# Performance work log

Hardware: AMD Instinct MI355X
Metric: run time of the kernel (lower is better)

The kernel has to match this reference:

```python
import jax, jax.numpy as jnp
import numpy as np

B, H, L, P = 16, 256, 8192, 64  # batch, d_input, seq_len, d_state


def setup_inputs() -> dict:
    key = jax.random.key(0)
    k1, k2, k3, k4, k5, k6 = jax.random.split(key, 6)
    u = jax.random.normal(k1, (B, H, L), dtype=jnp.float32)
    # diagonal SSM poles on an annulus inside the unit disk (stable discrete dynamics)
    radius = jax.random.uniform(k2, (P,), minval=0.5, maxval=0.99)
    theta = jax.random.uniform(k3, (P,), minval=0.0, maxval=2.0 * np.pi)
    A_re = (radius * jnp.cos(theta)).astype(jnp.float32)
    A_im = (radius * jnp.sin(theta)).astype(jnp.float32)
    # combined input/output mixing W = C*B, complex (H, P)
    BC_re = (jax.random.normal(k4, (H, P)) / np.sqrt(P)).astype(jnp.float32)
    BC_im = (jax.random.normal(k5, (H, P)) / np.sqrt(P)).astype(jnp.float32)
    # D skip vector: uniform_ring(min_radius=0.0, max_radius=1.0, field='real')
    D = jax.random.uniform(k6, (H,), minval=0.0, maxval=1.0, dtype=jnp.float32)
    return {"u": u, "A_re": A_re, "A_im": A_im, "BC_re": BC_re, "BC_im": BC_im, "D": D}


def reference(u, A_re, A_im, BC_re, BC_im, D):
    # Vandermonde kernel: k[h, l] = sum_p BC[h, p] * A[p]**l, computed stably via exp(l*log A)
    A = jax.lax.complex(A_re, A_im)                      # (P,)
    logA = jnp.log(A)                                    # (P,) complex
    ell = jnp.arange(L, dtype=jnp.float32)               # (L,)
    V = jnp.exp(logA[:, None] * ell[None, :])            # (P, L) complex Vandermonde
    BC = jax.lax.complex(BC_re, BC_im)                   # (H, P)
    k = jnp.einsum('hp,pl->hl', BC, V)                   # (H, L) complex kernel
    # circular FFT convolution (same-length fft/ifft as the torch code)
    u_s = jnp.fft.fft(u, axis=-1)                        # (B, H, L) complex
    k_s = jnp.fft.fft(k, axis=-1)                        # (H, L) complex
    y = jnp.fft.ifft(u_s * k_s[None, :, :], axis=-1).real
    y = y + D[None, :, None] * u                         # D*u skip
    return jnp.tanh(y)                                   # activation (dropout=0 -> identity)
```

## Files before the change

### kernel.cpp

```cpp
#include <hip/hip_runtime.h>
#include <cmath>


typedef _Float16 half8 __attribute__((ext_vector_type(8)));
typedef _Float16 half4v __attribute__((ext_vector_type(4)));
typedef float floatx16 __attribute__((ext_vector_type(16)));

#define NC 64
#define CM 128
#define ROWP 136
#define A2_BYTES ((size_t)256 * 128 * 256 * 2)
#define W_BYTES  ((size_t)128 * 128 * 2)
#define AM_OFF   (A2_BYTES + W_BYTES)

__device__ __forceinline__ float fast_tanh(float x) {
    float e2 = __expf(2.0f * x);
    return 1.0f - 2.0f / (e2 + 1.0f);
}

__global__ void fftconv_prep(const float* __restrict__ A_re, const float* __restrict__ A_im,
                             const float* __restrict__ BC_re, const float* __restrict__ BC_im,
                             const float* __restrict__ Dv, char* __restrict__ ws) {
    __shared__ float rr[64], th[64], br[64], bi[64];
    __shared__ float kk[CM];
    const int h = blockIdx.x, tid = threadIdx.x;
    if (tid < 64) {
        float x = A_re[tid], y = A_im[tid];
        rr[tid] = log2f(sqrtf(x * x + y * y));
        th[tid] = atan2f(y, x);
        br[tid] = BC_re[h * 64 + tid];
        bi[tid] = BC_im[h * 64 + tid];
    }
    __syncthreads();
    if (tid < CM) {
        float d = (float)tid, s = 0.f;
        for (int p = 0; p < 64; ++p) {
            float mag = exp2f(d * rr[p]);
            float ang = d * th[p];
            s += mag * (br[p] * cosf(ang) - bi[p] * sinf(ang));
        }
        kk[tid] = s;
    }
    __syncthreads();
    _Float16* A2 = (_Float16*)ws + (size_t)h * 128 * 256;
    const float Dh = Dv[h];
    for (int idx = tid; idx < 128 * 128; idx += 256) {
        int r = idx >> 7, pc = idx & 127, p = pc & 63;
        float e = (float)(r + 1);
        float mag = exp2f(e * rr[p]);
        float ang = e * th[p];
        float cr = mag * cosf(ang), ci = mag * sinf(ang);
        float val = (pc < 64) ? (br[p] * cr - bi[p] * ci) : -(br[p] * ci + bi[p] * cr);
        A2[r * 256 + pc] = (_Float16)val;
    }
    for (int idx = tid; idx < 128 * 128; idx += 256) {
        int r = idx >> 7, j = idx & 127;
        float v = (j <= r) ? kk[r - j] : 0.f;
        if (j == r) v += Dh;
        A2[r * 256 + CM + j] = (_Float16)v;
    }
    if (h == 0) {
        _Float16* W = (_Float16*)(ws + A2_BYTES);
        for (int idx = tid; idx < 128 * 128; idx += 256) {
            int pc = idx >> 7, j = idx & 127, p = pc & 63;
            float e = (float)(127 - j);
            float mag = exp2f(e * rr[p]);
            float ang = e * th[p];
            float v = (pc < 64) ? mag * cosf(ang) : mag * sinf(ang);
            W[pc * 128 + j] = (_Float16)v;
        }
        if (tid < 64) {
            float mag = exp2f(128.f * rr[tid]);
            float ang = 128.f * th[tid];
            float* aM = (float*)(ws + AM_OFF);
            aM[tid] = mag * cosf(ang);
            aM[64 + tid] = mag * sinf(ang);
        }
    }
}

__global__ __launch_bounds__(256, 2)
void fftconv_main(const float* __restrict__ u, const char* __restrict__ ws,
                  float* __restrict__ out) {
    __shared__ __align__(16) _Float16 u16p[NC * ROWP];
    __shared__ __align__(16) _Float16 S16[NC * ROWP];

    const int tid = threadIdx.x;
    const int lane = tid & 63;
    const int wv = tid >> 6;
    const int h = blockIdx.x >> 4;
    const int bb = blockIdx.x & 15;
    const float* ub = u + ((size_t)bb * 256 + h) * 8192;
    float* yb = out + ((size_t)bb * 256 + h) * 8192;

#pragma unroll
    for (int i = 0; i < 8; ++i) {
        int e4 = i * 256 + tid;
        float4 v = ((const float4*)ub)[e4];
        int el = e4 << 2;
        int c = el >> 7, j = el & 127;
        half4v hv = { (_Float16)v.x, (_Float16)v.y, (_Float16)v.z, (_Float16)v.w };
        *(half4v*)&u16p[c * ROWP + j] = hv;
    }
    __syncthreads();

    const int mrow = (wv << 5) + (lane & 31);
    const int kh = (lane >> 5) << 3;
    const int ncol = lane & 31;

    {
        const _Float16* Wg = (const _Float16*)(ws + A2_BYTES);
        floatx16 acc0 = {}; floatx16 acc1 = {};
#pragma unroll
        for (int s = 0; s < 8; ++s) {
            int k0 = (s << 4) + kh;
            half8 af = *(const half8*)(Wg + mrow * CM + k0);
            half8 b0 = *(const half8*)&u16p[ncol * ROWP + k0];
            half8 b1 = *(const half8*)&u16p[(ncol + 32) * ROWP + k0];
            acc0 = __builtin_amdgcn_mfma_f32_32x32x16_f16(af, b0, acc0, 0, 0, 0);
            acc1 = __builtin_amdgcn_mfma_f32_32x32x16_f16(af, b1, acc1, 0, 0, 0);
        }
        const int pc0 = (wv << 5) + ((lane >> 5) << 2);
#pragma unroll
        for (int g = 0; g < 4; ++g) {
            half4v h0 = { (_Float16)acc0[4 * g + 0], (_Float16)acc0[4 * g + 1],
                          (_Float16)acc0[4 * g + 2], (_Float16)acc0[4 * g + 3] };
            *(half4v*)&S16[ncol * ROWP + pc0 + 8 * g] = h0;
            half4v h1 = { (_Float16)acc1[4 * g + 0], (_Float16)acc1[4 * g + 1],
                          (_Float16)acc1[4 * g + 2], (_Float16)acc1[4 * g + 3] };
            *(half4v*)&S16[(ncol + 32) * ROWP + pc0 + 8 * g] = h1;
        }
    }
    __syncthreads();

    if (wv == 0) {
        const float* aM = (const float*)(ws + AM_OFF);
        const float amr = aM[lane], ami = aM[64 + lane];
        float sr = 0.f, si = 0.f;
#pragma unroll
        for (int c = NC - 8; c < NC; ++c) {
            float xr = (float)S16[c * ROWP + lane];
            float xi = (float)S16[c * ROWP + 64 + lane];
            float nr = fmaf(amr, sr, fmaf(-ami, si, xr));
            float ni = fmaf(amr, si, fmaf(ami, sr, xi));
            sr = nr; si = ni;
        }
#pragma unroll
        for (int c = 0; c < NC; ++c) {
            float xr = (float)S16[c * ROWP + lane];
            float xi = (float)S16[c * ROWP + 64 + lane];
            S16[c * ROWP + lane] = (_Float16)sr;
            S16[c * ROWP + 64 + lane] = (_Float16)si;
            float nr = fmaf(amr, sr, fmaf(-ami, si, xr));
            float ni = fmaf(amr, si, fmaf(ami, sr, xi));
            sr = nr; si = ni;
        }
    }
    __syncthreads();

    {
        const _Float16* Ag = (const _Float16*)ws + ((size_t)h * CM + mrow) * 256;
        floatx16 acc0 = {}; floatx16 acc1 = {};
#pragma unroll
        for (int s = 0; s < 8; ++s) {
            int k0 = (s << 4) + kh;
            half8 af = *(const half8*)(Ag + k0);
            half8 b0 = *(const half8*)&S16[ncol * ROWP + k0];
            half8 b1 = *(const half8*)&S16[(ncol + 32) * ROWP + k0];
            acc0 = __builtin_amdgcn_mfma_f32_32x32x16_f16(af, b0, acc0, 0, 0, 0);
            acc1 = __builtin_amdgcn_mfma_f32_32x32x16_f16(af, b1, acc1, 0, 0, 0);
        }
#pragma unroll
        for (int s = 0; s < 8; ++s) {
            int k0 = (s << 4) + kh;
            half8 af = *(const half8*)(Ag + CM + k0);
            half8 b0 = *(const half8*)&u16p[ncol * ROWP + k0];
            half8 b1 = *(const half8*)&u16p[(ncol + 32) * ROWP + k0];
            acc0 = __builtin_amdgcn_mfma_f32_32x32x16_f16(af, b0, acc0, 0, 0, 0);
            acc1 = __builtin_amdgcn_mfma_f32_32x32x16_f16(af, b1, acc1, 0, 0, 0);
        }
        const int r0 = (wv << 5) + ((lane >> 5) << 2);
#pragma unroll
        for (int g = 0; g < 4; ++g) {
            float4 o0;
            o0.x = fast_tanh(acc0[4 * g + 0]); o0.y = fast_tanh(acc0[4 * g + 1]);
            o0.z = fast_tanh(acc0[4 * g + 2]); o0.w = fast_tanh(acc0[4 * g + 3]);
            *(float4*)(yb + (size_t)ncol * CM + r0 + 8 * g) = o0;
            float4 o1;
            o1.x = fast_tanh(acc1[4 * g + 0]); o1.y = fast_tanh(acc1[4 * g + 1]);
            o1.z = fast_tanh(acc1[4 * g + 2]); o1.w = fast_tanh(acc1[4 * g + 3]);
            *(float4*)(yb + (size_t)(ncol + 32) * CM + r0 + 8 * g) = o1;
        }
    }
}

extern "C" void kernel_launch(void* const* d_in, const int* in_sizes, int n_in,
                              void* d_out, int out_size, void* d_ws, size_t ws_size,
                              hipStream_t stream) {
    const float* u     = (const float*)d_in[0];
    const float* A_re  = (const float*)d_in[1];
    const float* A_im  = (const float*)d_in[2];
    const float* BC_re = (const float*)d_in[3];
    const float* BC_im = (const float*)d_in[4];
    const float* Dv    = (const float*)d_in[5];
    float* out = (float*)d_out;
    char* ws = (char*)d_ws;

    hipLaunchKernelGGL(fftconv_prep, dim3(256), dim3(256), 0, stream,
                       A_re, A_im, BC_re, BC_im, Dv, ws);
    hipLaunchKernelGGL(fftconv_main, dim3(4096), dim3(256), 0, stream,
                       u, ws, out);
}
```

Before: 350.0 us.

## Parallelize chunk-state scan across all waves, swizzle LDS, prefetch weight fragments

The serial 64-step inter-chunk state recurrence, previously run by wave 0 alone, is split across all four waves. Each wave reconstructs its incoming state from the 8 preceding chunks using precomputed powers of A^128, then scans its own 16 chunks. LDS padding is replaced by an XOR swizzle to cut bank conflicts and LDS footprint. Global u loads and MFMA weight fragments are issued early into registers to overlap with LDS work, and launch bounds request 4 blocks per CU. The trade-offs are extra recurrence arithmetic and higher register pressure.

```diff
diff --git a/kernel.cpp b/kernel.cpp
--- a/kernel.cpp
+++ b/kernel.cpp
@@ -8,10 +8,11 @@
 
 #define NC 64
 #define CM 128
-#define ROWP 136
 #define A2_BYTES ((size_t)256 * 128 * 256 * 2)
 #define W_BYTES  ((size_t)128 * 128 * 2)
 #define AM_OFF   (A2_BYTES + W_BYTES)
+
+#define SWH(r, c) ((((r) << 7)) | ((c) ^ (((r) & 15) << 3)))
 
 __device__ __forceinline__ float fast_tanh(float x) {
     float e2 = __expf(2.0f * x);
@@ -79,11 +80,11 @@
     }
 }
 
-__global__ __launch_bounds__(256, 2)
+__global__ __launch_bounds__(256, 4)
 void fftconv_main(const float* __restrict__ u, const char* __restrict__ ws,
                   float* __restrict__ out) {
-    __shared__ __align__(16) _Float16 u16p[NC * ROWP];
-    __shared__ __align__(16) _Float16 S16[NC * ROWP];
+    __shared__ __align__(16) _Float16 u16[NC * CM];
+    __shared__ __align__(16) _Float16 S16[NC * CM];
 
     const int tid = threadIdx.x;
     const int lane = tid & 63;
@@ -93,91 +94,117 @@
     const float* ub = u + ((size_t)bb * 256 + h) * 8192;
     float* yb = out + ((size_t)bb * 256 + h) * 8192;
 
-#pragma unroll
-    for (int i = 0; i < 8; ++i) {
-        int e4 = i * 256 + tid;
-        float4 v = ((const float4*)ub)[e4];
-        int el = e4 << 2;
-        int c = el >> 7, j = el & 127;
-        half4v hv = { (_Float16)v.x, (_Float16)v.y, (_Float16)v.z, (_Float16)v.w };
-        *(half4v*)&u16p[c * ROWP + j] = hv;
-    }
-    __syncthreads();
-
     const int mrow = (wv << 5) + (lane & 31);
     const int kh = (lane >> 5) << 3;
     const int ncol = lane & 31;
 
+    const _Float16* Wg = (const _Float16*)(ws + A2_BYTES) + (size_t)mrow * CM + kh;
+    const _Float16* Ag = (const _Float16*)ws + ((size_t)h * CM + mrow) * 256 + kh;
+
+    float4 uv[8];
+#pragma unroll
+    for (int i = 0; i < 8; ++i) uv[i] = ((const float4*)ub)[i * 256 + tid];
+    half8 wf[8];
+#pragma unroll
+    for (int s = 0; s < 8; ++s) wf[s] = *(const half8*)(Wg + (s << 4));
+
+#pragma unroll
+    for (int i = 0; i < 8; ++i) {
+        int e4 = i * 256 + tid;
+        int c = e4 >> 5, j = (e4 << 2) & 127;
+        half4v hv = { (_Float16)uv[i].x, (_Float16)uv[i].y,
+                      (_Float16)uv[i].z, (_Float16)uv[i].w };
+        *(half4v*)&u16[SWH(c, j)] = hv;
+    }
+    __syncthreads();
+
     {
-        const _Float16* Wg = (const _Float16*)(ws + A2_BYTES);
         floatx16 acc0 = {}; floatx16 acc1 = {};
 #pragma unroll
         for (int s = 0; s < 8; ++s) {
             int k0 = (s << 4) + kh;
-            half8 af = *(const half8*)(Wg + mrow * CM + k0);
-            half8 b0 = *(const half8*)&u16p[ncol * ROWP + k0];
-            half8 b1 = *(const half8*)&u16p[(ncol + 32) * ROWP + k0];
-            acc0 = __builtin_amdgcn_mfma_f32_32x32x16_f16(af, b0, acc0, 0, 0, 0);
-            acc1 = __builtin_amdgcn_mfma_f32_32x32x16_f16(af, b1, acc1, 0, 0, 0);
+            half8 b0 = *(const half8*)&u16[SWH(ncol, k0)];
+            half8 b1 = *(const half8*)&u16[SWH(ncol + 32, k0)];
+            acc0 = __builtin_amdgcn_mfma_f32_32x32x16_f16(wf[s], b0, acc0, 0, 0, 0);
+            acc1 = __builtin_amdgcn_mfma_f32_32x32x16_f16(wf[s], b1, acc1, 0, 0, 0);
         }
         const int pc0 = (wv << 5) + ((lane >> 5) << 2);
 #pragma unroll
         for (int g = 0; g < 4; ++g) {
             half4v h0 = { (_Float16)acc0[4 * g + 0], (_Float16)acc0[4 * g + 1],
                           (_Float16)acc0[4 * g + 2], (_Float16)acc0[4 * g + 3] };
-            *(half4v*)&S16[ncol * ROWP + pc0 + 8 * g] = h0;
+            *(half4v*)&S16[SWH(ncol, pc0 + 8 * g)] = h0;
             half4v h1 = { (_Float16)acc1[4 * g + 0], (_Float16)acc1[4 * g + 1],
                           (_Float16)acc1[4 * g + 2], (_Float16)acc1[4 * g + 3] };
-            *(half4v*)&S16[(ncol + 32) * ROWP + pc0 + 8 * g] = h1;
-        }
-    }
-    __syncthreads();
-
-    if (wv == 0) {
+            *(half4v*)&S16[SWH(ncol + 32, pc0 + 8 * g)] = h1;
+        }
+    }
+    half8 gf[8];
+#pragma unroll
+    for (int s = 0; s < 8; ++s) gf[s] = *(const half8*)(Ag + (s << 4));
+    __syncthreads();
+
+    {
         const float* aM = (const float*)(ws + AM_OFF);
         const float amr = aM[lane], ami = aM[64 + lane];
+        float prd[8], pid[8];
+        prd[0] = 1.f; pid[0] = 0.f;
+#pragma unroll
+        for (int d = 1; d < 8; ++d) {
+            prd[d] = prd[d - 1] * amr - pid[d - 1] * ami;
+            pid[d] = prd[d - 1] * ami + pid[d - 1] * amr;
+        }
+        const int cbase = wv << 4;
         float sr = 0.f, si = 0.f;
 #pragma unroll
-        for (int c = NC - 8; c < NC; ++c) {
-            float xr = (float)S16[c * ROWP + lane];
-            float xi = (float)S16[c * ROWP + 64 + lane];
+        for (int d = 0; d < 8; ++d) {
+            int cc = (cbase - 1 - d) & 63;
+            float xr = (float)S16[SWH(cc, lane)];
+            float xi = (float)S16[SWH(cc, 64 + lane)];
+            sr = fmaf(prd[d], xr, fmaf(-pid[d], xi, sr));
+            si = fmaf(prd[d], xi, fmaf(pid[d], xr, si));
+        }
+        float er[16], ei[16];
+        er[0] = sr; ei[0] = si;
+#pragma unroll
+        for (int i = 1; i < 16; ++i) {
+            int cc = cbase + i - 1;
+            float xr = (float)S16[SWH(cc, lane)];
+            float xi = (float)S16[SWH(cc, 64 + lane)];
             float nr = fmaf(amr, sr, fmaf(-ami, si, xr));
             float ni = fmaf(amr, si, fmaf(ami, sr, xi));
-            sr = nr; si = ni;
-        }
-#pragma unroll
-        for (int c = 0; c < NC; ++c) {
-            float xr = (float)S16[c * ROWP + lane];
-            float xi = (float)S16[c * ROWP + 64 + lane];
-            S16[c * ROWP + lane] = (_Float16)sr;
-            S16[c * ROWP + 64 + lane] = (_Float16)si;
-            float nr = fmaf(amr, sr, fmaf(-ami, si, xr));
-            float ni = fmaf(amr, si, fmaf(ami, sr, xi));
-            sr = nr; si = ni;
-        }
-    }
+            sr = nr; si = ni; er[i] = sr; ei[i] = si;
+        }
+        __syncthreads();
+#pragma unroll
+        for (int i = 0; i < 16; ++i) {
+            int c = cbase + i;
+            S16[SWH(c, lane)] = (_Float16)er[i];
+            S16[SWH(c, 64 + lane)] = (_Float16)ei[i];
+        }
+    }
+    half8 tf[8];
+#pragma unroll
+    for (int s = 0; s < 8; ++s) tf[s] = *(const half8*)(Ag + CM + (s << 4));
     __syncthreads();
 
     {
-        const _Float16* Ag = (const _Float16*)ws + ((size_t)h * CM + mrow) * 256;
         floatx16 acc0 = {}; floatx16 acc1 = {};
 #pragma unroll
         for (int s = 0; s < 8; ++s) {
             int k0 = (s << 4) + kh;
-            half8 af = *(const half8*)(Ag + k0);
-            half8 b0 = *(const half8*)&S16[ncol * ROWP + k0];
-            half8 b1 = *(const half8*)&S16[(ncol + 32) * ROWP + k0];
-            acc0 = __builtin_amdgcn_mfma_f32_32x32x16_f16(af, b0, acc0, 0, 0, 0);
-            acc1 = __builtin_amdgcn_mfma_f32_32x32x16_f16(af, b1, acc1, 0, 0, 0);
+            half8 b0 = *(const half8*)&S16[SWH(ncol, k0)];
+            half8 b1 = *(const half8*)&S16[SWH(ncol + 32, k0)];
+            acc0 = __builtin_amdgcn_mfma_f32_32x32x16_f16(gf[s], b0, acc0, 0, 0, 0);
+            acc1 = __builtin_amdgcn_mfma_f32_32x32x16_f16(gf[s], b1, acc1, 0, 0, 0);
         }
 #pragma unroll
         for (int s = 0; s < 8; ++s) {
             int k0 = (s << 4) + kh;
-            half8 af = *(const half8*)(Ag + CM + k0);
-            half8 b0 = *(const half8*)&u16p[ncol * ROWP + k0];
-            half8 b1 = *(const half8*)&u16p[(ncol + 32) * ROWP + k0];
-            acc0 = __builtin_amdgcn_mfma_f32_32x32x16_f16(af, b0, acc0, 0, 0, 0);
-            acc1 = __builtin_amdgcn_mfma_f32_32x32x16_f16(af, b1, acc1, 0, 0, 0);
+            half8 b0 = *(const half8*)&u16[SWH(ncol, k0)];
+            half8 b1 = *(const half8*)&u16[SWH(ncol + 32, k0)];
+            acc0 = __builtin_amdgcn_mfma_f32_32x32x16_f16(tf[s], b0, acc0, 0, 0, 0);
+            acc1 = __builtin_amdgcn_mfma_f32_32x32x16_f16(tf[s], b1, acc1, 0, 0, 0);
         }
         const int r0 = (wv << 5) + ((lane >> 5) << 2);
 #pragma unroll
```

Result: faster. 333.9 us (-4.6%).
